# Kernel optimization log

Measured on AMD Instinct MI355X. Metric: run time of the kernel, lower is better.

Reference implementation:

```python
import jax, jax.numpy as jnp
import numpy as np

N_NODES = 100000


def _gcn_conv(x, W, b, src, dst):
    # PyG GCNConv: linear transform, symmetric-normalized scatter-add, bias.
    h = x @ W  # [N, d_out]
    ones = jnp.ones(src.shape[0], dtype=x.dtype)
    deg = jax.ops.segment_sum(ones, dst, num_segments=N_NODES)  # in-degree incl. self-loops
    dinv = jnp.where(deg > 0, jax.lax.rsqrt(deg), 0.0)
    norm = dinv[src] * dinv[dst]  # [E_tot]
    msg = h[src] * norm[:, None]  # [E_tot, d_out]
    out = jax.ops.segment_sum(msg, dst, num_segments=N_NODES)
    return out + b


def setup_inputs() -> dict:
    key = jax.random.key(0)
    ks = jax.random.split(key, 6)
    x = jax.random.normal(ks[0], (N_NODES, 128), dtype=jnp.float32)
    edge_index = jax.random.randint(ks[1], (2, 1600000), 0, N_NODES, dtype=jnp.int64)
    W1 = jax.random.normal(ks[2], (128, 128), dtype=jnp.float32) / np.sqrt(128.0)
    b1 = jnp.zeros((128,), dtype=jnp.float32)
    W2 = jax.random.normal(ks[3], (128, 64), dtype=jnp.float32) / np.sqrt(128.0)
    b2 = jnp.zeros((64,), dtype=jnp.float32)
    return {"x": x, "edge_index": edge_index, "W1": W1, "b1": b1, "W2": W2, "b2": b2}


def reference(x, edge_index, W1, b1, W2, b2):
    # Add self-loops (PyG GCNConv default add_self_loops=True)
    loops = jnp.arange(N_NODES, dtype=edge_index.dtype)
    src = jnp.concatenate([edge_index[0], loops])
    dst = jnp.concatenate([edge_index[1], loops])
    h = _gcn_conv(x, W1, b1, src, dst)
    h = jax.nn.relu(h)
    h = _gcn_conv(h, W2, b2, src, dst)
    return jax.nn.log_softmax(h, axis=1)
```

## Files before the change

### kernel.cpp

```cpp
#include <hip/hip_runtime.h>
#include <hip/hip_bf16.h>
#include <stdint.h>

#define N_NODES 100000
#define NBUCK 250
#define NPB   400
#define PTILE 4096
#define SEGCAP 8192

typedef short short8 __attribute__((ext_vector_type(8)));
typedef float floatx4 __attribute__((ext_vector_type(4)));

__device__ __forceinline__ unsigned short f2bf(float x) {
    uint32_t u = __float_as_uint(x);
    return (unsigned short)((u + 0x7fff + ((u >> 16) & 1)) >> 16);
}
__device__ __forceinline__ float bf2f(unsigned int h) {
    return __uint_as_float(h << 16);
}

__global__ __launch_bounds__(256) void convw_kernel(const float* __restrict__ W1,
                                                    unsigned short* __restrict__ Wt1h,
                                                    unsigned short* __restrict__ Wt1l,
                                                    const float* __restrict__ W2,
                                                    unsigned short* __restrict__ Wt2h,
                                                    unsigned short* __restrict__ Wt2l,
                                                    int* __restrict__ gCursor) {
    int i = blockIdx.x * 256 + threadIdx.x;
    if (i < 128 * 128) {
        int n = i >> 7, k = i & 127;
        float v = W1[k * 128 + n];
        unsigned short h = f2bf(v);
        Wt1h[i] = h;
        Wt1l[i] = f2bf(v - bf2f(h));
    } else if (i < 128 * 128 + 64 * 128) {
        int j = i - 128 * 128;
        int n = j >> 7, k = j & 127;
        float v = W2[k * 64 + n];
        unsigned short h = f2bf(v);
        Wt2h[j] = h;
        Wt2l[j] = f2bf(v - bf2f(h));
    }
    if (blockIdx.x == 0 && threadIdx.x < NBUCK) gCursor[threadIdx.x] = 0;
}

__global__ __launch_bounds__(256) void partition_kernel(const int* __restrict__ src,
                                                        const int* __restrict__ dst,
                                                        int* __restrict__ gCursor,
                                                        unsigned* __restrict__ pairs, int E) {
    __shared__ int hist[NBUCK], toffs[NBUCK], gb[NBUCK], lpos[NBUCK];
    __shared__ int sm[256];
    __shared__ unsigned pairbuf[PTILE];
    __shared__ int gidx[PTILE];
    int tid = threadIdx.x;
    int ntiles = (E + PTILE - 1) / PTILE;
    for (int tile = blockIdx.x; tile < ntiles; tile += gridDim.x) {
        int base = tile * PTILE;
        int n = min(PTILE, E - base);
        for (int i = tid; i < NBUCK; i += 256) { hist[i] = 0; lpos[i] = 0; }
        __syncthreads();
        unsigned epk[16]; int eb[16];
#pragma unroll
        for (int k = 0; k < 16; ++k) {
            int e = base + k * 256 + tid;
            if (e < base + n) {
                unsigned d = (unsigned)dst[e];
                eb[k] = (int)(d / NPB);
                epk[k] = ((unsigned)src[e] << 9) | (d - (unsigned)eb[k] * NPB);
                atomicAdd(&hist[eb[k]], 1);
            } else eb[k] = -1;
        }
        __syncthreads();
        int v = (tid < NBUCK) ? hist[tid] : 0;
        sm[tid] = v;
        __syncthreads();
#pragma unroll
        for (int off = 1; off < 256; off <<= 1) {
            int t = (tid >= off) ? sm[tid - off] : 0;
            __syncthreads();
            sm[tid] += t;
            __syncthreads();
        }
        if (tid < NBUCK) {
            toffs[tid] = sm[tid] - v;
            if (v > 0) gb[tid] = atomicAdd(&gCursor[tid], v);
        }
        __syncthreads();
#pragma unroll
        for (int k = 0; k < 16; ++k) {
            int b = eb[k];
            if (b >= 0) {
                int p = toffs[b] + atomicAdd(&lpos[b], 1);
                pairbuf[p] = epk[k];
                int rel = gb[b] + (p - toffs[b]);
                gidx[p] = (rel < SEGCAP) ? (b * SEGCAP + rel) : -1;
            }
        }
        __syncthreads();
        for (int i = tid; i < n; i += 256) {
            int gi = gidx[i];
            if (gi >= 0) pairs[gi] = pairbuf[i];
        }
        __syncthreads();
    }
}

__global__ __launch_bounds__(256) void bucket_csr_kernel(const unsigned* __restrict__ pairs,
                                                         const int* __restrict__ gCursor,
                                                         int* __restrict__ adj,
                                                         int* __restrict__ offsB,
                                                         int* __restrict__ offsE,
                                                         float* __restrict__ dinv) {
    __shared__ int hist[NPB], excl[NPB], cursor[NPB];
    __shared__ int ladj[SEGCAP];
    __shared__ int sm[256];
    int b = blockIdx.x, tid = threadIdx.x;
    int nodeBase = b * NPB;
    int segBase = b * SEGCAP;
    int cnt = min(gCursor[b], SEGCAP);
    for (int i = tid; i < NPB; i += 256) hist[i] = 0;
    __syncthreads();
    for (int i = tid; i < cnt; i += 256)
        atomicAdd(&hist[pairs[segBase + i] & 511u], 1);
    __syncthreads();
    int total = 0;
    for (int r = 0; r < 2; ++r) {
        int idx = r * 256 + tid;
        int v = (idx < NPB) ? hist[idx] : 0;
        sm[tid] = v;
        __syncthreads();
#pragma unroll
        for (int off = 1; off < 256; off <<= 1) {
            int t = (tid >= off) ? sm[tid - off] : 0;
            __syncthreads();
            sm[tid] += t;
            __syncthreads();
        }
        if (idx < NPB) {
            int e = total + sm[tid] - v;
            excl[idx] = e;
            cursor[idx] = e;
        }
        total += sm[255];
        __syncthreads();
    }
    for (int j = tid; j < NPB; j += 256) {
        offsB[nodeBase + j] = segBase + excl[j];
        offsE[nodeBase + j] = segBase + excl[j] + hist[j];
        dinv[nodeBase + j] = rsqrtf((float)hist[j] + 1.0f);
    }
    __syncthreads();
    for (int i = tid; i < cnt; i += 256) {
        unsigned p = pairs[segBase + i];
        int pos = atomicAdd(&cursor[p & 511u], 1);
        if (pos < SEGCAP) ladj[pos] = (int)(p >> 9);
    }
    __syncthreads();
    for (int i = tid; i < cnt; i += 256) adj[segBase + i] = ladj[i];
}

__device__ __forceinline__ void split8(const float* p, short8& h, short8& l) {
    float4 a = *(const float4*)p;
    float4 b = *(const float4*)(p + 4);
    float v[8] = {a.x, a.y, a.z, a.w, b.x, b.y, b.z, b.w};
#pragma unroll
    for (int i = 0; i < 8; ++i) {
        unsigned short hh = f2bf(v[i]);
        h[i] = (short)hh;
        l[i] = (short)f2bf(v[i] - bf2f(hh));
    }
}

template <int N, bool SPLIT_IN>
__global__ __launch_bounds__(256) void gemm_mfma_kernel(
    const float* __restrict__ Af,
    const unsigned short* __restrict__ Ah, const unsigned short* __restrict__ Al,
    const unsigned short* __restrict__ WtH, const unsigned short* __restrict__ WtL,
    const float* __restrict__ dinv,
    unsigned short* __restrict__ Ch, int nrows) {
    constexpr int NT = N / 16;
    __shared__ char Wl[2 * N * 256];
    int tid = threadIdx.x;
    {
        const char* s0 = (const char*)WtH;
        const char* s1 = (const char*)WtL;
        const int chunks = N * 16;
        for (int i = tid; i < 2 * chunks; i += 256) {
            int buf = (i >= chunks) ? 1 : 0;
            int c = i - buf * chunks;
            int nn = c >> 4;
            float4 v = *(const float4*)((buf ? s1 : s0) + c * 16);
            int dstoff = (c * 16) ^ ((nn & 7) << 4);
            *(float4*)(Wl + buf * (N * 256) + dstoff) = v;
        }
    }
    __syncthreads();

    int wid = tid >> 6, lane = tid & 63;
    int rowbase = blockIdx.x * 128 + wid * 32;
    int lr = lane & 15, lg = lane >> 4;

    floatx4 acc[2][NT] = {};
    for (int ks = 0; ks < 4; ++ks) {
        short8 afh[2], afl[2];
#pragma unroll
        for (int rt = 0; rt < 2; ++rt) {
            int r = rowbase + rt * 16 + lr;
            if (r > nrows - 1) r = nrows - 1;
            size_t off = (size_t)r * 128 + ks * 32 + (lg << 3);
            if (SPLIT_IN) {
                split8(Af + off, afh[rt], afl[rt]);
            } else {
                afh[rt] = *(const short8*)(Ah + off);
                afl[rt] = *(const short8*)(Al + off);
            }
        }
#pragma unroll
        for (int t = 0; t < NT; ++t) {
            int nn = t * 16 + lr;
            int off = (nn * 256 + ks * 64 + (lg << 4)) ^ ((nn & 7) << 4);
            short8 bh = *(const short8*)(Wl + off);
            short8 bl = *(const short8*)(Wl + N * 256 + off);
#pragma unroll
            for (int rt = 0; rt < 2; ++rt) {
                acc[rt][t] = __builtin_amdgcn_mfma_f32_16x16x32_bf16(afh[rt], bh, acc[rt][t], 0, 0, 0);
                acc[rt][t] = __builtin_amdgcn_mfma_f32_16x16x32_bf16(afl[rt], bh, acc[rt][t], 0, 0, 0);
                acc[rt][t] = __builtin_amdgcn_mfma_f32_16x16x32_bf16(afh[rt], bl, acc[rt][t], 0, 0, 0);
            }
        }
    }
#pragma unroll
    for (int rt = 0; rt < 2; ++rt) {
#pragma unroll
        for (int j = 0; j < 4; ++j) {
            int row = rowbase + rt * 16 + lg * 4 + j;
            if (row >= nrows) continue;
            float dv = dinv[row];
#pragma unroll
            for (int t = 0; t < NT; ++t) {
                int col = t * 16 + lr;
                Ch[(size_t)row * N + col] = f2bf(acc[rt][t][j] * dv);
            }
        }
    }
}

__global__ __launch_bounds__(256) void gather128_kernel(
    const unsigned short* __restrict__ hh,
    const int* __restrict__ offsB, const int* __restrict__ offsE,
    const int* __restrict__ adj,
    const float* __restrict__ dinv, const float* __restrict__ b,
    unsigned short* __restrict__ gh, unsigned short* __restrict__ gl, int n) {
    int wid = threadIdx.x >> 6, lane = threadIdx.x & 63;
    int r = blockIdx.x * 4 + wid;
    if (r >= n) return;
    float dr = dinv[r];
    uint32_t vh = *(const uint32_t*)(hh + (size_t)r * 128 + 2 * lane);
    float a0x = bf2f(vh & 0xffffu);
    float a0y = bf2f(vh >> 16);
    float a1x = 0.f, a1y = 0.f, a2x = 0.f, a2y = 0.f, a3x = 0.f, a3y = 0.f;
    int e0 = offsB[r], e1 = offsE[r];
    int j = e0;
    for (; j + 4 <= e1; j += 4) {
        int s0 = adj[j], s1 = adj[j + 1], s2 = adj[j + 2], s3 = adj[j + 3];
        uint32_t u0 = *(const uint32_t*)(hh + (size_t)s0 * 128 + 2 * lane);
        uint32_t u1 = *(const uint32_t*)(hh + (size_t)s1 * 128 + 2 * lane);
        uint32_t u2 = *(const uint32_t*)(hh + (size_t)s2 * 128 + 2 * lane);
        uint32_t u3 = *(const uint32_t*)(hh + (size_t)s3 * 128 + 2 * lane);
        a0x += bf2f(u0 & 0xffffu); a0y += bf2f(u0 >> 16);
        a1x += bf2f(u1 & 0xffffu); a1y += bf2f(u1 >> 16);
        a2x += bf2f(u2 & 0xffffu); a2y += bf2f(u2 >> 16);
        a3x += bf2f(u3 & 0xffffu); a3y += bf2f(u3 >> 16);
    }
    for (; j < e1; ++j) {
        int s = adj[j];
        uint32_t u = *(const uint32_t*)(hh + (size_t)s * 128 + 2 * lane);
        a0x += bf2f(u & 0xffffu); a0y += bf2f(u >> 16);
    }
    float accx = (a0x + a1x) + (a2x + a3x);
    float accy = (a0y + a1y) + (a2y + a3y);
    accx = fmaxf(fmaf(accx, dr, b[2 * lane]), 0.f);
    accy = fmaxf(fmaf(accy, dr, b[2 * lane + 1]), 0.f);
    unsigned short hx = f2bf(accx), hy = f2bf(accy);
    *(uint32_t*)(gh + (size_t)r * 128 + 2 * lane) = (uint32_t)hx | ((uint32_t)hy << 16);
    unsigned short lx = f2bf(accx - bf2f(hx)), ly = f2bf(accy - bf2f(hy));
    *(uint32_t*)(gl + (size_t)r * 128 + 2 * lane) = (uint32_t)lx | ((uint32_t)ly << 16);
}

__global__ __launch_bounds__(256) void gather64_lsm_kernel(
    const unsigned short* __restrict__ hh,
    const int* __restrict__ offsB, const int* __restrict__ offsE,
    const int* __restrict__ adj,
    const float* __restrict__ dinv, const float* __restrict__ b,
    float* __restrict__ out, int n) {
    int wid = threadIdx.x >> 6, lane = threadIdx.x & 63;
    int r = blockIdx.x * 4 + wid;
    if (r >= n) return;
    float dr = dinv[r];
    float a0 = bf2f(hh[(size_t)r * 64 + lane]);
    float a1 = 0.f, a2 = 0.f, a3 = 0.f;
    int e0 = offsB[r], e1 = offsE[r];
    int j = e0;
    for (; j + 4 <= e1; j += 4) {
        int s0 = adj[j], s1 = adj[j + 1], s2 = adj[j + 2], s3 = adj[j + 3];
        a0 += bf2f(hh[(size_t)s0 * 64 + lane]);
        a1 += bf2f(hh[(size_t)s1 * 64 + lane]);
        a2 += bf2f(hh[(size_t)s2 * 64 + lane]);
        a3 += bf2f(hh[(size_t)s3 * 64 + lane]);
    }
    for (; j < e1; ++j) a0 += bf2f(hh[(size_t)adj[j] * 64 + lane]);
    float acc = (a0 + a1) + (a2 + a3);
    float v = fmaf(acc, dr, b[lane]);
    float m = v;
#pragma unroll
    for (int off = 32; off; off >>= 1) m = fmaxf(m, __shfl_xor(m, off));
    float ex = __expf(v - m);
    float sum = ex;
#pragma unroll
    for (int off = 32; off; off >>= 1) sum += __shfl_xor(sum, off);
    out[(size_t)r * 64 + lane] = v - m - __logf(sum);
}

extern "C" void kernel_launch(void* const* d_in, const int* in_sizes, int n_in,
                              void* d_out, int out_size, void* d_ws, size_t ws_size,
                              hipStream_t stream) {
    const float* x  = (const float*)d_in[0];
    const int*   ei = (const int*)d_in[1];
    const float* W1 = (const float*)d_in[2];
    const float* b1 = (const float*)d_in[3];
    const float* W2 = (const float*)d_in[4];
    const float* b2 = (const float*)d_in[5];
    float* out = (float*)d_out;

    const int N = N_NODES;
    const int E = in_sizes[1] / 2;
    const int* src = ei;
    const int* dst = ei + E;

    char* ws = (char*)d_ws;
    float* dinv   = (float*)(ws + 0x000000ll);
    int* offsB    = (int*)  (ws + 0x080000ll);
    int* offsE    = (int*)  (ws + 0x100000ll);
    int* gCursor  = (int*)  (ws + 0x180000ll);
    unsigned short* Wt1h = (unsigned short*)(ws + 0x190000ll);
    unsigned short* Wt1l = (unsigned short*)(ws + 0x198000ll);
    unsigned short* Wt2h = (unsigned short*)(ws + 0x1A0000ll);
    unsigned short* Wt2l = (unsigned short*)(ws + 0x1A4000ll);
    int* adj      = (int*)  (ws + (2ll << 20));
    unsigned short* g1h = (unsigned short*)(ws + (11ll << 20));
    unsigned short* g1l = (unsigned short*)(ws + (37ll << 20));
    unsigned short* h1h = (unsigned short*)(ws + (63ll << 20));
    unsigned* pairs = (unsigned*)h1h;
    unsigned short* h2h = h1h;

    convw_kernel<<<(128 * 128 + 64 * 128 + 255) / 256, 256, 0, stream>>>(
        W1, Wt1h, Wt1l, W2, Wt2h, Wt2l, gCursor);

    int ntiles = (E + PTILE - 1) / PTILE;
    partition_kernel<<<ntiles, 256, 0, stream>>>(src, dst, gCursor, pairs, E);
    bucket_csr_kernel<<<NBUCK, 256, 0, stream>>>(pairs, gCursor, adj, offsB, offsE, dinv);

    const int GB = (N + 127) / 128;

    gemm_mfma_kernel<128, true><<<GB, 256, 0, stream>>>(
        x, nullptr, nullptr, Wt1h, Wt1l, dinv, h1h, N);

    gather128_kernel<<<(N + 3) / 4, 256, 0, stream>>>(h1h, offsB, offsE, adj, dinv, b1,
                                                      g1h, g1l, N);

    gemm_mfma_kernel<64, false><<<GB, 256, 0, stream>>>(
        nullptr, g1h, g1l, Wt2h, Wt2l, dinv, h2h, N);

    gather64_lsm_kernel<<<(N + 3) / 4, 256, 0, stream>>>(h2h, offsB, offsE, adj, dinv, b2, out, N);
}
```

Baseline: 232.8 us.

## Fuse edge partitioning with first GEMM and move source normalization into gather

The first GEMM no longer needs dinv. Source-degree scaling moves into the layer-1 gather, which reads dinv per neighbor. This lets the partition pass and the x@W1 GEMM run as disjoint block ranges of one launch, with W1 split/transposed in shared memory per block. The W2 conversion runs as extra blocks of the CSR build kernel, the cursor reset becomes a memset, and launches drop from seven to five. Cost: an extra random dinv load per edge in the gather, and W1 conversion repeated in every GEMM block.

```diff
diff --git a/kernel.cpp b/kernel.cpp
--- a/kernel.cpp
+++ b/kernel.cpp
@@ -19,102 +19,169 @@
     return __uint_as_float(h << 16);
 }
 
-__global__ __launch_bounds__(256) void convw_kernel(const float* __restrict__ W1,
-                                                    unsigned short* __restrict__ Wt1h,
-                                                    unsigned short* __restrict__ Wt1l,
-                                                    const float* __restrict__ W2,
-                                                    unsigned short* __restrict__ Wt2h,
-                                                    unsigned short* __restrict__ Wt2l,
-                                                    int* __restrict__ gCursor) {
-    int i = blockIdx.x * 256 + threadIdx.x;
-    if (i < 128 * 128) {
-        int n = i >> 7, k = i & 127;
-        float v = W1[k * 128 + n];
-        unsigned short h = f2bf(v);
-        Wt1h[i] = h;
-        Wt1l[i] = f2bf(v - bf2f(h));
-    } else if (i < 128 * 128 + 64 * 128) {
-        int j = i - 128 * 128;
-        int n = j >> 7, k = j & 127;
-        float v = W2[k * 64 + n];
-        unsigned short h = f2bf(v);
-        Wt2h[j] = h;
-        Wt2l[j] = f2bf(v - bf2f(h));
-    }
-    if (blockIdx.x == 0 && threadIdx.x < NBUCK) gCursor[threadIdx.x] = 0;
-}
-
-__global__ __launch_bounds__(256) void partition_kernel(const int* __restrict__ src,
-                                                        const int* __restrict__ dst,
-                                                        int* __restrict__ gCursor,
-                                                        unsigned* __restrict__ pairs, int E) {
-    __shared__ int hist[NBUCK], toffs[NBUCK], gb[NBUCK], lpos[NBUCK];
-    __shared__ int sm[256];
-    __shared__ unsigned pairbuf[PTILE];
-    __shared__ int gidx[PTILE];
+__device__ __forceinline__ void split8(const float* p, short8& h, short8& l) {
+    float4 a = *(const float4*)p;
+    float4 b = *(const float4*)(p + 4);
+    float v[8] = {a.x, a.y, a.z, a.w, b.x, b.y, b.z, b.w};
+#pragma unroll
+    for (int i = 0; i < 8; ++i) {
+        unsigned short hh = f2bf(v[i]);
+        h[i] = (short)hh;
+        l[i] = (short)f2bf(v[i] - bf2f(hh));
+    }
+}
+
+struct PartSh {
+    int hist[NBUCK], toffs[NBUCK], gb[NBUCK], lpos[NBUCK];
+    int sm[256];
+    unsigned pairbuf[PTILE];
+    int gidx[PTILE];
+};
+struct GemmSh {
+    char Wl[2 * 128 * 256];
+};
+
+__global__ __launch_bounds__(256) void fusedA_kernel(
+    const int* __restrict__ src, const int* __restrict__ dst,
+    int* __restrict__ gCursor, unsigned* __restrict__ pairs, int E, int npart,
+    const float* __restrict__ x, const float* __restrict__ W1,
+    unsigned short* __restrict__ h1h, int nrows) {
+    __shared__ union { PartSh p; GemmSh g; } sh;
     int tid = threadIdx.x;
-    int ntiles = (E + PTILE - 1) / PTILE;
-    for (int tile = blockIdx.x; tile < ntiles; tile += gridDim.x) {
-        int base = tile * PTILE;
-        int n = min(PTILE, E - base);
-        for (int i = tid; i < NBUCK; i += 256) { hist[i] = 0; lpos[i] = 0; }
+
+    if ((int)blockIdx.x < npart) {
+        int ntiles = (E + PTILE - 1) / PTILE;
+        for (int tile = blockIdx.x; tile < ntiles; tile += npart) {
+            int base = tile * PTILE;
+            int n = min(PTILE, E - base);
+            for (int i = tid; i < NBUCK; i += 256) { sh.p.hist[i] = 0; sh.p.lpos[i] = 0; }
+            __syncthreads();
+            unsigned epk[16]; int eb[16];
+#pragma unroll
+            for (int k = 0; k < 16; ++k) {
+                int e = base + k * 256 + tid;
+                if (e < base + n) {
+                    unsigned d = (unsigned)dst[e];
+                    eb[k] = (int)(d / NPB);
+                    epk[k] = ((unsigned)src[e] << 9) | (d - (unsigned)eb[k] * NPB);
+                    atomicAdd(&sh.p.hist[eb[k]], 1);
+                } else eb[k] = -1;
+            }
+            __syncthreads();
+            int v = (tid < NBUCK) ? sh.p.hist[tid] : 0;
+            sh.p.sm[tid] = v;
+            __syncthreads();
+#pragma unroll
+            for (int off = 1; off < 256; off <<= 1) {
+                int t = (tid >= off) ? sh.p.sm[tid - off] : 0;
+                __syncthreads();
+                sh.p.sm[tid] += t;
+                __syncthreads();
+            }
+            if (tid < NBUCK) {
+                sh.p.toffs[tid] = sh.p.sm[tid] - v;
+                if (v > 0) sh.p.gb[tid] = atomicAdd(&gCursor[tid], v);
+            }
+            __syncthreads();
+#pragma unroll
+            for (int k = 0; k < 16; ++k) {
+                int b = eb[k];
+                if (b >= 0) {
+                    int p = sh.p.toffs[b] + atomicAdd(&sh.p.lpos[b], 1);
+                    sh.p.pairbuf[p] = epk[k];
+                    int rel = sh.p.gb[b] + (p - sh.p.toffs[b]);
+                    sh.p.gidx[p] = (rel < SEGCAP) ? (b * SEGCAP + rel) : -1;
+                }
+            }
+            __syncthreads();
+            for (int i = tid; i < n; i += 256) {
+                int gi = sh.p.gidx[i];
+                if (gi >= 0) pairs[gi] = sh.p.pairbuf[i];
+            }
+            __syncthreads();
+        }
+    } else {
+        {
+            int n = tid & 127, kh = (tid >> 7) << 6;
+            for (int kc = 0; kc < 64; kc += 8) {
+                short8 h8, l8;
+#pragma unroll
+                for (int q = 0; q < 8; ++q) {
+                    float v = W1[(kh + kc + q) * 128 + n];
+                    unsigned short hv = f2bf(v);
+                    h8[q] = (short)hv;
+                    l8[q] = (short)f2bf(v - bf2f(hv));
+                }
+                int off = (n * 256 + (kh + kc) * 2) ^ ((n & 7) << 4);
+                *(short8*)(sh.g.Wl + off) = h8;
+                *(short8*)(sh.g.Wl + 128 * 256 + off) = l8;
+            }
+        }
         __syncthreads();
-        unsigned epk[16]; int eb[16];
-#pragma unroll
-        for (int k = 0; k < 16; ++k) {
-            int e = base + k * 256 + tid;
-            if (e < base + n) {
-                unsigned d = (unsigned)dst[e];
-                eb[k] = (int)(d / NPB);
-                epk[k] = ((unsigned)src[e] << 9) | (d - (unsigned)eb[k] * NPB);
-                atomicAdd(&hist[eb[k]], 1);
-            } else eb[k] = -1;
-        }
-        __syncthreads();
-        int v = (tid < NBUCK) ? hist[tid] : 0;
-        sm[tid] = v;
-        __syncthreads();
-#pragma unroll
-        for (int off = 1; off < 256; off <<= 1) {
-            int t = (tid >= off) ? sm[tid - off] : 0;
-            __syncthreads();
-            sm[tid] += t;
-            __syncthreads();
-        }
-        if (tid < NBUCK) {
-            toffs[tid] = sm[tid] - v;
-            if (v > 0) gb[tid] = atomicAdd(&gCursor[tid], v);
-        }
-        __syncthreads();
-#pragma unroll
-        for (int k = 0; k < 16; ++k) {
-            int b = eb[k];
-            if (b >= 0) {
-                int p = toffs[b] + atomicAdd(&lpos[b], 1);
-                pairbuf[p] = epk[k];
-                int rel = gb[b] + (p - toffs[b]);
-                gidx[p] = (rel < SEGCAP) ? (b * SEGCAP + rel) : -1;
-            }
-        }
-        __syncthreads();
-        for (int i = tid; i < n; i += 256) {
-            int gi = gidx[i];
-            if (gi >= 0) pairs[gi] = pairbuf[i];
-        }
-        __syncthreads();
-    }
-}
-
-__global__ __launch_bounds__(256) void bucket_csr_kernel(const unsigned* __restrict__ pairs,
-                                                         const int* __restrict__ gCursor,
-                                                         int* __restrict__ adj,
-                                                         int* __restrict__ offsB,
-                                                         int* __restrict__ offsE,
-                                                         float* __restrict__ dinv) {
+
+        int wid = tid >> 6, lane = tid & 63;
+        int rowbase = ((int)blockIdx.x - npart) * 128 + wid * 32;
+        int lr = lane & 15, lg = lane >> 4;
+
+        floatx4 acc[2][8] = {};
+        for (int ks = 0; ks < 4; ++ks) {
+            short8 afh[2], afl[2];
+#pragma unroll
+            for (int rt = 0; rt < 2; ++rt) {
+                int r = rowbase + rt * 16 + lr;
+                if (r > nrows - 1) r = nrows - 1;
+                split8(x + (size_t)r * 128 + ks * 32 + (lg << 3), afh[rt], afl[rt]);
+            }
+#pragma unroll
+            for (int t = 0; t < 8; ++t) {
+                int nn = t * 16 + lr;
+                int off = (nn * 256 + ks * 64 + (lg << 4)) ^ ((nn & 7) << 4);
+                short8 bh = *(const short8*)(sh.g.Wl + off);
+                short8 bl = *(const short8*)(sh.g.Wl + 128 * 256 + off);
+#pragma unroll
+                for (int rt = 0; rt < 2; ++rt) {
+                    acc[rt][t] = __builtin_amdgcn_mfma_f32_16x16x32_bf16(afh[rt], bh, acc[rt][t], 0, 0, 0);
+                    acc[rt][t] = __builtin_amdgcn_mfma_f32_16x16x32_bf16(afl[rt], bh, acc[rt][t], 0, 0, 0);
+                    acc[rt][t] = __builtin_amdgcn_mfma_f32_16x16x32_bf16(afh[rt], bl, acc[rt][t], 0, 0, 0);
+                }
+            }
+        }
+#pragma unroll
+        for (int rt = 0; rt < 2; ++rt) {
+#pragma unroll
+            for (int j = 0; j < 4; ++j) {
+                int row = rowbase + rt * 16 + lg * 4 + j;
+                if (row >= nrows) continue;
+#pragma unroll
+                for (int t = 0; t < 8; ++t)
+                    h1h[(size_t)row * 128 + t * 16 + lr] = f2bf(acc[rt][t][j]);
+            }
+        }
+    }
+}
+
+__global__ __launch_bounds__(256) void fusedB_kernel(
+    const unsigned* __restrict__ pairs, const int* __restrict__ gCursor,
+    int* __restrict__ adj, int* __restrict__ offsB, int* __restrict__ offsE,
+    float* __restrict__ dinv,
+    const float* __restrict__ W2, unsigned short* __restrict__ Wt2h,
+    unsigned short* __restrict__ Wt2l) {
     __shared__ int hist[NPB], excl[NPB], cursor[NPB];
     __shared__ int ladj[SEGCAP];
     __shared__ int sm[256];
-    int b = blockIdx.x, tid = threadIdx.x;
+    int tid = threadIdx.x;
+    if ((int)blockIdx.x >= NBUCK) {
+        int j = ((int)blockIdx.x - NBUCK) * 256 + tid;
+        if (j < 64 * 128) {
+            int n = j >> 7, k = j & 127;
+            float v = W2[k * 64 + n];
+            unsigned short h = f2bf(v);
+            Wt2h[j] = h;
+            Wt2l[j] = f2bf(v - bf2f(h));
+        }
+        return;
+    }
+    int b = blockIdx.x;
     int nodeBase = b * NPB;
     int segBase = b * SEGCAP;
     int cnt = min(gCursor[b], SEGCAP);
@@ -159,39 +226,24 @@
     for (int i = tid; i < cnt; i += 256) adj[segBase + i] = ladj[i];
 }
 
-__device__ __forceinline__ void split8(const float* p, short8& h, short8& l) {
-    float4 a = *(const float4*)p;
-    float4 b = *(const float4*)(p + 4);
-    float v[8] = {a.x, a.y, a.z, a.w, b.x, b.y, b.z, b.w};
-#pragma unroll
-    for (int i = 0; i < 8; ++i) {
-        unsigned short hh = f2bf(v[i]);
-        h[i] = (short)hh;
-        l[i] = (short)f2bf(v[i] - bf2f(hh));
-    }
-}
-
-template <int N, bool SPLIT_IN>
-__global__ __launch_bounds__(256) void gemm_mfma_kernel(
-    const float* __restrict__ Af,
+__global__ __launch_bounds__(256) void gemm64_kernel(
     const unsigned short* __restrict__ Ah, const unsigned short* __restrict__ Al,
     const unsigned short* __restrict__ WtH, const unsigned short* __restrict__ WtL,
     const float* __restrict__ dinv,
     unsigned short* __restrict__ Ch, int nrows) {
-    constexpr int NT = N / 16;
-    __shared__ char Wl[2 * N * 256];
+    __shared__ char Wl[2 * 64 * 256];
     int tid = threadIdx.x;
     {
         const char* s0 = (const char*)WtH;
         const char* s1 = (const char*)WtL;
-        const int chunks = N * 16;
+        const int chunks = 64 * 16;
         for (int i = tid; i < 2 * chunks; i += 256) {
             int buf = (i >= chunks) ? 1 : 0;
             int c = i - buf * chunks;
             int nn = c >> 4;
             float4 v = *(const float4*)((buf ? s1 : s0) + c * 16);
             int dstoff = (c * 16) ^ ((nn & 7) << 4);
-            *(float4*)(Wl + buf * (N * 256) + dstoff) = v;
+            *(float4*)(Wl + buf * (64 * 256) + dstoff) = v;
         }
     }
     __syncthreads();
@@ -200,7 +252,7 @@
     int rowbase = blockIdx.x * 128 + wid * 32;
     int lr = lane & 15, lg = lane >> 4;
 
-    floatx4 acc[2][NT] = {};
+    floatx4 acc[2][4] = {};
     for (int ks = 0; ks < 4; ++ks) {
         short8 afh[2], afl[2];
 #pragma unroll
@@ -208,19 +260,15 @@
             int r = rowbase + rt * 16 + lr;
             if (r > nrows - 1) r = nrows - 1;
             size_t off = (size_t)r * 128 + ks * 32 + (lg << 3);
-            if (SPLIT_IN) {
-                split8(Af + off, afh[rt], afl[rt]);
-            } else {
-                afh[rt] = *(const short8*)(Ah + off);
-                afl[rt] = *(const short8*)(Al + off);
-            }
-        }
-#pragma unroll
-        for (int t = 0; t < NT; ++t) {
+            afh[rt] = *(const short8*)(Ah + off);
+            afl[rt] = *(const short8*)(Al + off);
+        }
+#pragma unroll
+        for (int t = 0; t < 4; ++t) {
             int nn = t * 16 + lr;
             int off = (nn * 256 + ks * 64 + (lg << 4)) ^ ((nn & 7) << 4);
             short8 bh = *(const short8*)(Wl + off);
-            short8 bl = *(const short8*)(Wl + N * 256 + off);
+            short8 bl = *(const short8*)(Wl + 64 * 256 + off);
 #pragma unroll
             for (int rt = 0; rt < 2; ++rt) {
                 acc[rt][t] = __builtin_amdgcn_mfma_f32_16x16x32_bf16(afh[rt], bh, acc[rt][t], 0, 0, 0);
@@ -237,10 +285,8 @@
             if (row >= nrows) continue;
             float dv = dinv[row];
 #pragma unroll
-            for (int t = 0; t < NT; ++t) {
-                int col = t * 16 + lr;
-                Ch[(size_t)row * N + col] = f2bf(acc[rt][t][j] * dv);
-            }
+            for (int t = 0; t < 4; ++t)
+                Ch[(size_t)row * 64 + t * 16 + lr] = f2bf(acc[rt][t][j] * dv);
         }
     }
 }
@@ -256,26 +302,29 @@
     if (r >= n) return;
     float dr = dinv[r];
     uint32_t vh = *(const uint32_t*)(hh + (size_t)r * 128 + 2 * lane);
-    float a0x = bf2f(vh & 0xffffu);
-    float a0y = bf2f(vh >> 16);
+    float a0x = dr * bf2f(vh & 0xffffu);
+    float a0y = dr * bf2f(vh >> 16);
     float a1x = 0.f, a1y = 0.f, a2x = 0.f, a2y = 0.f, a3x = 0.f, a3y = 0.f;
     int e0 = offsB[r], e1 = offsE[r];
     int j = e0;
     for (; j + 4 <= e1; j += 4) {
         int s0 = adj[j], s1 = adj[j + 1], s2 = adj[j + 2], s3 = adj[j + 3];
+        float d0 = dinv[s0], d1 = dinv[s1], d2 = dinv[s2], d3 = dinv[s3];
         uint32_t u0 = *(const uint32_t*)(hh + (size_t)s0 * 128 + 2 * lane);
         uint32_t u1 = *(const uint32_t*)(hh + (size_t)s1 * 128 + 2 * lane);
         uint32_t u2 = *(const uint32_t*)(hh + (size_t)s2 * 128 + 2 * lane);
         uint32_t u3 = *(const uint32_t*)(hh + (size_t)s3 * 128 + 2 * lane);
-        a0x += bf2f(u0 & 0xffffu); a0y += bf2f(u0 >> 16);
-        a1x += bf2f(u1 & 0xffffu); a1y += bf2f(u1 >> 16);
-        a2x += bf2f(u2 & 0xffffu); a2y += bf2f(u2 >> 16);
-        a3x += bf2f(u3 & 0xffffu); a3y += bf2f(u3 >> 16);
+        a0x = fmaf(bf2f(u0 & 0xffffu), d0, a0x); a0y = fmaf(bf2f(u0 >> 16), d0, a0y);
+        a1x = fmaf(bf2f(u1 & 0xffffu), d1, a1x); a1y = fmaf(bf2f(u1 >> 16), d1, a1y);
+        a2x = fmaf(bf2f(u2 & 0xffffu), d2, a2x); a2y = fmaf(bf2f(u2 >> 16), d2, a2y);
+        a3x = fmaf(bf2f(u3 & 0xffffu), d3, a3x); a3y = fmaf(bf2f(u3 >> 16), d3, a3y);
     }
     for (; j < e1; ++j) {
         int s = adj[j];
+        float ds = dinv[s];
         uint32_t u = *(const uint32_t*)(hh + (size_t)s * 128 + 2 * lane);
-        a0x += bf2f(u & 0xffffu); a0y += bf2f(u >> 16);
+        a0x = fmaf(bf2f(u & 0xffffu), ds, a0x);
+        a0y = fmaf(bf2f(u >> 16), ds, a0y);
     }
     float accx = (a0x + a1x) + (a2x + a3x);
     float accy = (a0y + a1y) + (a2y + a3y);
@@ -342,34 +391,31 @@
     int* offsB    = (int*)  (ws + 0x080000ll);
     int* offsE    = (int*)  (ws + 0x100000ll);
     int* gCursor  = (int*)  (ws + 0x180000ll);
-    unsigned short* Wt1h = (unsigned short*)(ws + 0x190000ll);
-    unsigned short* Wt1l = (unsigned short*)(ws + 0x198000ll);
-    unsigned short* Wt2h = (unsigned short*)(ws + 0x1A0000ll);
-    unsigned short* Wt2l = (unsigned short*)(ws + 0x1A4000ll);
-    int* adj      = (int*)  (ws + (2ll << 20));
-    unsigned short* g1h = (unsigned short*)(ws + (11ll << 20));
-    unsigned short* g1l = (unsigned short*)(ws + (37ll << 20));
-    unsigned short* h1h = (unsigned short*)(ws + (63ll << 20));
-    unsigned* pairs = (unsigned*)h1h;
-    unsigned short* h2h = h1h;
-
-    convw_kernel<<<(128 * 128 + 64 * 128 + 255) / 256, 256, 0, stream>>>(
-        W1, Wt1h, Wt1l, W2, Wt2h, Wt2l, gCursor);
-
-    int ntiles = (E + PTILE - 1) / PTILE;
-    partition_kernel<<<ntiles, 256, 0, stream>>>(src, dst, gCursor, pairs, E);
-    bucket_csr_kernel<<<NBUCK, 256, 0, stream>>>(pairs, gCursor, adj, offsB, offsE, dinv);
-
-    const int GB = (N + 127) / 128;
-
-    gemm_mfma_kernel<128, true><<<GB, 256, 0, stream>>>(
-        x, nullptr, nullptr, Wt1h, Wt1l, dinv, h1h, N);
-
-    gather128_kernel<<<(N + 3) / 4, 256, 0, stream>>>(h1h, offsB, offsE, adj, dinv, b1,
-                                                      g1h, g1l, N);
-
-    gemm_mfma_kernel<64, false><<<GB, 256, 0, stream>>>(
-        nullptr, g1h, g1l, Wt2h, Wt2l, dinv, h2h, N);
-
-    gather64_lsm_kernel<<<(N + 3) / 4, 256, 0, stream>>>(h2h, offsB, offsE, adj, dinv, b2, out, N);
-}
+    unsigned short* Wt2h = (unsigned short*)(ws + 0x190000ll);
+    unsigned short* Wt2l = (unsigned short*)(ws + 0x1A0000ll);
+    int* adj      = (int*)  (ws + (2ll  << 20));
+    unsigned* pairs = (unsigned*)(ws + (11ll << 20));
+    unsigned short* g1h = (unsigned short*)(ws + (20ll << 20));
+    unsigned short* g1l = (unsigned short*)(ws + (46ll << 20));
+    unsigned short* h1h = (unsigned short*)(ws + (72ll << 20));
+    unsigned short* h2h = (unsigned short*)(ws + (98ll << 20));
+
+    const int npart = (E + PTILE - 1) / PTILE;
+    const int ngemm = (N + 127) / 128;
+
+    hipMemsetAsync(gCursor, 0, NBUCK * sizeof(int), stream);
+
+    fusedA_kernel<<<npart + ngemm, 256, 0, stream>>>(
+        src, dst, gCursor, pairs, E, npart, x, W1, h1h, N);
+
+    fusedB_kernel<<<NBUCK + (64 * 128 + 255) / 256, 256, 0, stream>>>(
+        pairs, gCursor, adj, offsB, offsE, dinv, W2, Wt2h, Wt2l);
+
+    gather128_kernel<<<(N + 3) / 4, 256, 0, stream>>>(
+        h1h, offsB, offsE, adj, dinv, b1, g1h, g1l, N);
+
+    gemm64_kernel<<<ngemm, 256, 0, stream>>>(g1h, g1l, Wt2h, Wt2l, dinv, h2h, N);
+
+    gather64_lsm_kernel<<<(N + 3) / 4, 256, 0, stream>>>(
+        h2h, offsB, offsE, adj, dinv, b2, out, N);
+}
```

Result: faster. 228.0 us (-2.1%).
